# Kernel tuning notes

Measured on AMD Instinct MI355X. Metric: run time of the kernel, lower is better.

## Reference

```python
import jax, jax.numpy as jnp
import numpy as np

TEMPERATURE = 0.75
SINKHORN_ITERS = 7
EPS = 1e-6
R_THRESH = 1e-3


def setup_inputs() -> dict:
    key = jax.random.key(0)
    k1, k2, k3, k4 = jax.random.split(key, 4)
    b, h, t, d = 1, 8, 2048, 64
    n = 32  # uniform buckets of size t // n = 64
    q = jax.random.normal(k1, (b, h, t, d), jnp.float32)
    k_ = jax.random.normal(k2, (b, h, t, d), jnp.float32)
    v = jax.random.normal(k3, (b, h, t, d), jnp.float32)
    gumbel_u = jax.random.uniform(k4, (b * h, n, n), jnp.float32)
    return {"q": q, "k": k_, "v": v, "gumbel_u": gumbel_u, "num_buckets": n}


def _sort_net_R(qm, km, gumbel_u, d):
    # qm, km: [bh, n, s, d] -> bucket sums [bh, n, d]
    q_sums = qm.sum(axis=2)
    k_sums = km.sum(axis=2)
    logits = jnp.einsum('bie,bje->bij', q_sums, k_sums) * (d ** -0.5)
    # gumbel_sinkhorn(relu(logits))
    r = jnp.log(jax.nn.relu(logits) + EPS)
    g = -jnp.log(-jnp.log(gumbel_u + EPS) + EPS)
    r = (r + g) / TEMPERATURE
    for _ in range(SINKHORN_ITERS):
        r = r - jax.nn.logsumexp(r, axis=2, keepdims=True)
        r = r - jax.nn.logsumexp(r, axis=1, keepdims=True)
    return jnp.exp(r)  # [bh, n, n]


def reference(q, k, v, gumbel_u, num_buckets):
    b, h, t, d = q.shape
    bh = b * h
    n = num_buckets
    s = t // n  # uniform bucket size
    qm = q.reshape(bh, n, s, d)
    km = k.reshape(bh, n, s, d)
    vm = v.reshape(bh, n, s, d)

    R = _sort_net_R(qm, km, gumbel_u, d)
    # torch skips pairs with R_ij <= 1e-3 (output is zero); multiply by masked R
    Rm = jnp.where(R > R_THRESH, R, 0.0)

    scale = d ** -0.5
    # keys for pair (i, j) are concat(k_i, k_j): split score into self + cross
    S_self = jnp.einsum('bise,bite->bist', qm, km) * scale          # [bh,n,s,s]
    S_cross = jnp.einsum('bise,bjte->bijst', qm, km) * scale        # [bh,n,n,s,s]
    scores = jnp.concatenate(
        [jnp.broadcast_to(S_self[:, :, None], (bh, n, n, s, s)), S_cross],
        axis=-1)                                                    # [bh,n,n,s,2s]
    w = jax.nn.softmax(scores, axis=-1)
    w_i, w_j = w[..., :s], w[..., s:]
    # out_ij = (w_i @ v_i + w_j @ v_j) * R_ij, summed over j
    out = (jnp.einsum('bijst,bite,bij->bise', w_i, vm, Rm)
           + jnp.einsum('bijst,bjte,bij->bise', w_j, vm, Rm))       # [bh,n,s,d]
    return out.reshape(b, h, t, d)
```

## Files before the change

kernel.cpp:

```cpp
#include <hip/hip_runtime.h>
#include <math.h>
#include <stdint.h>

#define BH 8
#define NB 32
#define SS 64
#define DD 64
#define TT 2048

typedef float f32x16 __attribute__((ext_vector_type(16)));
typedef short bf16x8 __attribute__((ext_vector_type(8)));
typedef unsigned short u16;

__device__ __forceinline__ unsigned pkbf(float a, float b) {
  unsigned r;
  asm("v_cvt_pk_bf16_f32 %0, %1, %2" : "=v"(r) : "v"(a), "v"(b));
  return r;
}
__device__ __forceinline__ float exp2x(float x) {
  float r;
  asm("v_exp_f32 %0, %1" : "=v"(r) : "v"(x));
  return r;
}
__device__ __forceinline__ float log2x(float x) {
  float r;
  asm("v_log_f32 %0, %1" : "=v"(r) : "v"(x));
  return r;
}
__device__ __forceinline__ bf16x8 pack8v(const f32x16& v, const int b) {
  union { unsigned u[4]; bf16x8 v8; } x;
  x.u[0] = pkbf(v[b + 0], v[b + 1]);
  x.u[1] = pkbf(v[b + 2], v[b + 3]);
  x.u[2] = pkbf(v[b + 4], v[b + 5]);
  x.u[3] = pkbf(v[b + 6], v[b + 7]);
  return x.v8;
}

__global__ __launch_bounds__(256) void prep_kernel(
    const float* __restrict__ q, const float* __restrict__ k, const float* __restrict__ v,
    u16* __restrict__ qb, u16* __restrict__ kb, u16* __restrict__ vtb,
    float* __restrict__ qsum, float* __restrict__ ksum)
{
  __shared__ float qt[64][68];
  __shared__ float kt[64][68];
  __shared__ float vt[64][68];

  const int T = blockIdx.x;
  const int t = threadIdx.x;
  const float* qsrc = q + (size_t)T * 4096;
  const float* ksrc = k + (size_t)T * 4096;
  const float* vsrc = v + (size_t)T * 4096;

#pragma unroll
  for (int r4 = 0; r4 < 4; ++r4) {
    int f = r4 * 256 + t;
    int row = f >> 4, c4 = (f & 15) << 2;
    *(float4*)&qt[row][c4] = ((const float4*)qsrc)[f];
    *(float4*)&kt[row][c4] = ((const float4*)ksrc)[f];
    *(float4*)&vt[row][c4] = ((const float4*)vsrc)[f];
  }
  __syncthreads();

  const float qscale = 0.18033688011112042f;

#pragma unroll
  for (int half = 0; half < 2; ++half) {
    int x = half * 256 + t;
    int c = x >> 6, lane = x & 63;
    int l31 = lane & 31, hi = lane >> 5;
    int m = c >> 2, s = c & 3;
    int row = l31 + 32 * m;
    int cb = 16 * s + 4 * hi;
    float4 a = *(const float4*)&qt[row][cb];
    float4 b = *(const float4*)&qt[row][cb + 8];
    uint4 o;
    o.x = pkbf(a.x * qscale, a.y * qscale);
    o.y = pkbf(a.z * qscale, a.w * qscale);
    o.z = pkbf(b.x * qscale, b.y * qscale);
    o.w = pkbf(b.z * qscale, b.w * qscale);
    *(uint4*)(qb + (size_t)T * 4096 + (size_t)x * 8) = o;

    float4 ka = *(const float4*)&kt[row][cb];
    float4 kb4 = *(const float4*)&kt[row][cb + 8];
    uint4 ko;
    ko.x = pkbf(ka.x, ka.y);
    ko.y = pkbf(ka.z, ka.w);
    ko.z = pkbf(kb4.x, kb4.y);
    ko.w = pkbf(kb4.z, kb4.w);
    *(uint4*)(kb + (size_t)T * 4096 + (size_t)x * 8) = ko;

    int d = l31 + 32 * m;
    int kb0 = 16 * s + 4 * hi;
    uint4 vo;
    vo.x = pkbf(vt[kb0 + 0][d], vt[kb0 + 1][d]);
    vo.y = pkbf(vt[kb0 + 2][d], vt[kb0 + 3][d]);
    vo.z = pkbf(vt[kb0 + 8][d], vt[kb0 + 9][d]);
    vo.w = pkbf(vt[kb0 + 10][d], vt[kb0 + 11][d]);
    *(uint4*)(vtb + (size_t)T * 4096 + (size_t)x * 8) = vo;
  }

  if (t < 64) {
    float s = 0.f;
#pragma unroll 8
    for (int r = 0; r < 64; ++r) s += qt[r][t];
    qsum[T * 64 + t] = s;
  } else if (t < 128) {
    int c = t - 64;
    float s = 0.f;
#pragma unroll 8
    for (int r = 0; r < 64; ++r) s += kt[r][c];
    ksum[T * 64 + c] = s;
  }
}

__global__ __launch_bounds__(512) void attn_kernel(
    const u16* __restrict__ qb, const u16* __restrict__ kb,
    const u16* __restrict__ vtb, const float* __restrict__ qsum,
    const float* __restrict__ ksum, const float* __restrict__ gu,
    float* __restrict__ out)
{
  __shared__ __align__(16) unsigned char smem[35840];
  float (*redh)[2][32][68] = (float (*)[2][32][68])smem;
  float (*cbuf)[32] = (float (*)[32])(smem + 34816);
  float* qs    = (float*)smem;
  float* ks    = qs + 32 * 65;
  float* rbufS = ks + 32 * 65;
  float* colb  = rbufS + 32 * 33;
  float* RmRow = colb + 32;

  const int bh  = blockIdx.x & 7;
  const int i   = blockIdx.x >> 3;
  const int t   = threadIdx.x;
  const int w   = t >> 6;
  const int n   = w & 1;
  const int g   = w >> 1;
  const int lane = t & 63;
  const int l31 = lane & 31;
  const int hi  = lane >> 5;

  const u16* qtile = qb + ((size_t)(bh * NB + i)) * 4096;
  const u16* kbh   = kb + (size_t)bh * NB * 4096;
  const u16* vbh   = vtb + (size_t)bh * NB * 4096;

#define LOADG(dst, base)                                                      \
  {                                                                           \
    _Pragma("unroll") for (int m = 0; m < 2; ++m)                             \
    _Pragma("unroll") for (int s = 0; s < 4; ++s)                             \
      dst[m][s] = *(const bf16x8*)((base) + ((size_t)((m * 4 + s) * 64 + lane)) * 8); \
  }

  bf16x8 qB[4];
#pragma unroll
  for (int s = 0; s < 4; ++s)
    qB[s] = *(const bf16x8*)(qtile + ((size_t)((n * 4 + s) * 64 + lane)) * 8);

  float rij8[8];
  {
    const float L2E = 1.4426950408889634f;
    const float LN2 = 0.6931471805599453f;

    {
      int idx = t * 4;
      float4 qv = *(const float4*)(qsum + bh * 2048 + idx);
      float4 kv = *(const float4*)(ksum + bh * 2048 + idx);
      int b = idx >> 6, e = idx & 63;
      float* qd = qs + b * 65 + e;
      qd[0] = qv.x; qd[1] = qv.y; qd[2] = qv.z; qd[3] = qv.w;
      float* kd = ks + b * 65 + e;
      kd[0] = kv.x; kd[1] = kv.y; kd[2] = kv.z; kd[3] = kv.w;
    }
    __syncthreads();

    const int G = t >> 5;
    const int j = t & 31;
    float rr2[2];
#pragma unroll
    for (int x = 0; x < 2; ++x) {
      int ii = G + 16 * x;
      float acc = 0.f;
      for (int e = 0; e < 64; ++e) acc += qs[ii * 65 + e] * ks[j * 65 + e];
      acc *= 0.125f;
      float u = gu[bh * 1024 + ii * 32 + j];
      float gg = -logf(-logf(u + 1e-6f) + 1e-6f);
      rr2[x] = (logf(fmaxf(acc, 0.f) + 1e-6f) + gg) * (1.0f / 0.75f);
    }

    for (int it = 0; it < 7; ++it) {
#pragma unroll
      for (int x = 0; x < 2; ++x) {
        float s = exp2x(rr2[x] * L2E);
        s += __shfl_xor(s, 16, 32);
        s += __shfl_xor(s, 8, 32);
        s += __shfl_xor(s, 4, 32);
        s += __shfl_xor(s, 2, 32);
        s += __shfl_xor(s, 1, 32);
        rr2[x] -= log2x(fmaxf(s, 1e-30f)) * LN2;
      }
#pragma unroll
      for (int x = 0; x < 2; ++x) rbufS[(G + 16 * x) * 33 + j] = rr2[x];
      __syncthreads();
#pragma unroll
      for (int x = 0; x < 2; ++x) {
        int col = G + 16 * x;
        float s2 = exp2x(rbufS[j * 33 + col] * L2E);
        s2 += __shfl_xor(s2, 16, 32);
        s2 += __shfl_xor(s2, 8, 32);
        s2 += __shfl_xor(s2, 4, 32);
        s2 += __shfl_xor(s2, 2, 32);
        s2 += __shfl_xor(s2, 1, 32);
        if (j == 0) colb[col] = log2x(fmaxf(s2, 1e-30f)) * LN2;
      }
      __syncthreads();
#pragma unroll
      for (int x = 0; x < 2; ++x) rr2[x] -= colb[j];
    }

#pragma unroll
    for (int x = 0; x < 2; ++x) {
      if (G + 16 * x == i) {
        float R = exp2x(rr2[x] * L2E);
        RmRow[j] = (R > 1e-3f) ? R : 0.f;
      }
    }
    __syncthreads();
#pragma unroll
    for (int jj = 0; jj < 8; ++jj) rij8[jj] = RmRow[g + 4 * jj];
  }

  bf16x8 kA[2][4], vB[2][4];
  LOADG(kA, kbh + (size_t)g * 4096);
  LOADG(vB, vbh + (size_t)g * 4096);

  float m0, S0;
  bf16x8 psA[4];
  {
    const u16* kib = kbh + (size_t)i * 4096;
    bf16x8 kAi[2][4];
    LOADG(kAi, kib);
    f32x16 aS0, aS1;
#pragma unroll
    for (int r = 0; r < 16; ++r) { aS0[r] = 0.f; aS1[r] = 0.f; }
#pragma unroll
    for (int s = 0; s < 4; ++s) {
      aS0 = __builtin_amdgcn_mfma_f32_32x32x16_bf16(kAi[0][s], qB[s], aS0, 0, 0, 0);
      aS1 = __builtin_amdgcn_mfma_f32_32x32x16_bf16(kAi[1][s], qB[s], aS1, 0, 0, 0);
    }
    float mx[16];
#pragma unroll
    for (int r = 0; r < 16; ++r) mx[r] = fmaxf(aS0[r], aS1[r]);
#pragma unroll
    for (int off = 8; off > 0; off >>= 1)
#pragma unroll
      for (int r = 0; r < off; ++r) mx[r] = fmaxf(mx[r], mx[r + off]);
    float mm = fmaxf(mx[0], __shfl_xor(mx[0], 32, 64));
#pragma unroll
    for (int r = 0; r < 16; ++r) { aS0[r] = exp2x(aS0[r] - mm); aS1[r] = exp2x(aS1[r] - mm); }
    float sm[16];
#pragma unroll
    for (int r = 0; r < 16; ++r) sm[r] = aS0[r] + aS1[r];
#pragma unroll
    for (int off = 8; off > 0; off >>= 1)
#pragma unroll
      for (int r = 0; r < off; ++r) sm[r] += sm[r + off];
    S0 = sm[0] + __shfl_xor(sm[0], 32, 64);
    m0 = mm;
    psA[0] = pack8v(aS0, 0);
    psA[1] = pack8v(aS0, 8);
    psA[2] = pack8v(aS1, 0);
    psA[3] = pack8v(aS1, 8);
  }

  f32x16 outAcc[2];
#pragma unroll
  for (int nv = 0; nv < 2; ++nv)
#pragma unroll
    for (int e = 0; e < 16; ++e) outAcc[nv][e] = 0.f;
  float cacc = 0.f;

#pragma unroll
  for (int jj = 0; jj < 8; ++jj) {
    const int j = g + 4 * jj;
    const float rij = rij8[jj];

    f32x16 a0, a1;
#pragma unroll
    for (int r = 0; r < 16; ++r) { a0[r] = 0.f; a1[r] = 0.f; }
    __builtin_amdgcn_s_setprio(1);
#pragma unroll
    for (int s = 0; s < 4; ++s) {
      a0 = __builtin_amdgcn_mfma_f32_32x32x16_bf16(kA[0][s], qB[s], a0, 0, 0, 0);
      a1 = __builtin_amdgcn_mfma_f32_32x32x16_bf16(kA[1][s], qB[s], a1, 0, 0, 0);
    }
    __builtin_amdgcn_s_setprio(0);

    if (jj < 7) LOADG(kA, kbh + (size_t)(j + 4) * 4096);

    float mx[16];
#pragma unroll
    for (int r = 0; r < 16; ++r) mx[r] = fmaxf(a0[r], a1[r]);
#pragma unroll
    for (int off = 8; off > 0; off >>= 1)
#pragma unroll
      for (int r = 0; r < off; ++r) mx[r] = fmaxf(mx[r], mx[r + off]);
    float mc = fmaxf(mx[0], __shfl_xor(mx[0], 32, 64));
    float mj = fmaxf(m0, mc);
#pragma unroll
    for (int r = 0; r < 16; ++r) { a0[r] = exp2x(a0[r] - mj); a1[r] = exp2x(a1[r] - mj); }
    float sm[16];
#pragma unroll
    for (int r = 0; r < 16; ++r) sm[r] = a0[r] + a1[r];
#pragma unroll
    for (int off = 8; off > 0; off >>= 1)
#pragma unroll
      for (int r = 0; r < off; ++r) sm[r] += sm[r + off];
    float ssum = sm[0] + __shfl_xor(sm[0], 32, 64);
    float e0 = exp2x(m0 - mj);
    float den = S0 * e0 + ssum;
    float inv = rij / den;
    cacc += e0 * inv;
#pragma unroll
    for (int r = 0; r < 16; ++r) { a0[r] *= inv; a1[r] *= inv; }

    __builtin_amdgcn_s_setprio(1);
#pragma unroll
    for (int s = 0; s < 4; ++s) {
      bf16x8 wf = (s < 2) ? pack8v(a0, 8 * (s & 1)) : pack8v(a1, 8 * (s & 1));
      outAcc[0] = __builtin_amdgcn_mfma_f32_32x32x16_bf16(wf, vB[0][s], outAcc[0], 0, 0, 0);
      outAcc[1] = __builtin_amdgcn_mfma_f32_32x32x16_bf16(wf, vB[1][s], outAcc[1], 0, 0, 0);
    }
    __builtin_amdgcn_s_setprio(0);

    if (jj < 7) LOADG(vB, vbh + (size_t)(j + 4) * 4096);
  }

  {
    const u16* vib = vbh + (size_t)i * 4096;
    bf16x8 vBi[2][4];
    LOADG(vBi, vib);
    f32x16 U[2];
#pragma unroll
    for (int nv = 0; nv < 2; ++nv)
#pragma unroll
      for (int e = 0; e < 16; ++e) U[nv][e] = 0.f;
#pragma unroll
    for (int s = 0; s < 4; ++s) {
      U[0] = __builtin_amdgcn_mfma_f32_32x32x16_bf16(psA[s], vBi[0][s], U[0], 0, 0, 0);
      U[1] = __builtin_amdgcn_mfma_f32_32x32x16_bf16(psA[s], vBi[1][s], U[1], 0, 0, 0);
    }
    if (hi == 0) cbuf[w][l31] = cacc;
    __syncthreads();
#pragma unroll
    for (int r = 0; r < 16; ++r) {
      int row = (r & 3) + 8 * (r >> 2) + 4 * hi;
      float cr = cbuf[w][row];
      outAcc[0][r] += U[0][r] * cr;
      outAcc[1][r] += U[1][r] * cr;
    }
  }

#define RED_W(buf)                                                         \
  {                                                                        \
    _Pragma("unroll") for (int ne = 0; ne < 2; ++ne)                       \
    _Pragma("unroll") for (int r = 0; r < 16; ++r) {                       \
      int row = (r & 3) + 8 * (r >> 2) + 4 * hi;                           \
      (buf)[row][l31 + 32 * ne] = outAcc[ne][r];                           \
    }                                                                      \
  }
#define RED_A(buf)                                                         \
  {                                                                        \
    _Pragma("unroll") for (int ne = 0; ne < 2; ++ne)                       \
    _Pragma("unroll") for (int r = 0; r < 16; ++r) {                       \
      int row = (r & 3) + 8 * (r >> 2) + 4 * hi;                           \
      outAcc[ne][r] += (buf)[row][l31 + 32 * ne];                          \
    }                                                                      \
  }

  if (g >= 2) RED_W(redh[n][g - 2]);
  __syncthreads();
  if (g < 2) RED_A(redh[n][g]);
  __syncthreads();
  if (g == 1) RED_W(redh[n][0]);
  __syncthreads();
  if (g == 0) {
    RED_A(redh[n][0]);
    RED_W(redh[n][0]);
  }
  __syncthreads();

  {
    int row = t >> 3;
    int nr = row >> 5, lrow = row & 31;
    int col0 = (t & 7) * 8;
    float4 a = *(const float4*)&redh[nr][0][lrow][col0];
    float4 b = *(const float4*)&redh[nr][0][lrow][col0 + 4];
    float* ob = out + ((size_t)bh * TT + i * SS + row) * DD + col0;
    *(float4*)ob = a;
    *(float4*)(ob + 4) = b;
  }
#undef LOADG
#undef RED_W
#undef RED_A
}

extern "C" void kernel_launch(void* const* d_in, const int* in_sizes, int n_in,
                              void* d_out, int out_size, void* d_ws, size_t ws_size,
                              hipStream_t stream) {
  (void)in_sizes; (void)n_in; (void)out_size; (void)ws_size;
  const float* q  = (const float*)d_in[0];
  const float* k  = (const float*)d_in[1];
  const float* v  = (const float*)d_in[2];
  const float* gu = (const float*)d_in[3];
  float* out = (float*)d_out;

  char* wsb = (char*)d_ws;
  u16* qb   = (u16*)(wsb);
  u16* kb   = (u16*)(wsb + (1 << 21));
  u16* vtb  = (u16*)(wsb + (2 << 21));
  float* qsum = (float*)(wsb + (3 << 21));
  float* ksum = (float*)(wsb + (3 << 21) + (1 << 16));

  prep_kernel<<<256, 256, 0, stream>>>(q, k, v, qb, kb, vtb, qsum, ksum);
  attn_kernel<<<BH * NB, 512, 0, stream>>>(qb, kb, vtb, qsum, ksum, gu, out);
}
```

Before: 34.26 us.

## Compute Sinkhorn matrix once per head in extra prep blocks instead of per attention block

Measured after the change: 48.44 us. +41.4%, slower.

```diff
diff --git a/kernel.cpp b/kernel.cpp
--- a/kernel.cpp
+++ b/kernel.cpp
@@ -38,95 +38,185 @@
 
 __global__ __launch_bounds__(256) void prep_kernel(
     const float* __restrict__ q, const float* __restrict__ k, const float* __restrict__ v,
+    const float* __restrict__ gu,
     u16* __restrict__ qb, u16* __restrict__ kb, u16* __restrict__ vtb,
-    float* __restrict__ qsum, float* __restrict__ ksum)
+    float* __restrict__ qsum, float* __restrict__ ksum, float* __restrict__ Rm)
 {
-  __shared__ float qt[64][68];
-  __shared__ float kt[64][68];
-  __shared__ float vt[64][68];
-
-  const int T = blockIdx.x;
+  __shared__ float smemF[3][64][68];
+
+  const int bid = blockIdx.x;
   const int t = threadIdx.x;
-  const float* qsrc = q + (size_t)T * 4096;
-  const float* ksrc = k + (size_t)T * 4096;
-  const float* vsrc = v + (size_t)T * 4096;
-
-#pragma unroll
-  for (int r4 = 0; r4 < 4; ++r4) {
-    int f = r4 * 256 + t;
-    int row = f >> 4, c4 = (f & 15) << 2;
-    *(float4*)&qt[row][c4] = ((const float4*)qsrc)[f];
-    *(float4*)&kt[row][c4] = ((const float4*)ksrc)[f];
-    *(float4*)&vt[row][c4] = ((const float4*)vsrc)[f];
-  }
-  __syncthreads();
-
-  const float qscale = 0.18033688011112042f;
-
-#pragma unroll
-  for (int half = 0; half < 2; ++half) {
-    int x = half * 256 + t;
-    int c = x >> 6, lane = x & 63;
-    int l31 = lane & 31, hi = lane >> 5;
-    int m = c >> 2, s = c & 3;
-    int row = l31 + 32 * m;
-    int cb = 16 * s + 4 * hi;
-    float4 a = *(const float4*)&qt[row][cb];
-    float4 b = *(const float4*)&qt[row][cb + 8];
-    uint4 o;
-    o.x = pkbf(a.x * qscale, a.y * qscale);
-    o.y = pkbf(a.z * qscale, a.w * qscale);
-    o.z = pkbf(b.x * qscale, b.y * qscale);
-    o.w = pkbf(b.z * qscale, b.w * qscale);
-    *(uint4*)(qb + (size_t)T * 4096 + (size_t)x * 8) = o;
-
-    float4 ka = *(const float4*)&kt[row][cb];
-    float4 kb4 = *(const float4*)&kt[row][cb + 8];
-    uint4 ko;
-    ko.x = pkbf(ka.x, ka.y);
-    ko.y = pkbf(ka.z, ka.w);
-    ko.z = pkbf(kb4.x, kb4.y);
-    ko.w = pkbf(kb4.z, kb4.w);
-    *(uint4*)(kb + (size_t)T * 4096 + (size_t)x * 8) = ko;
-
-    int d = l31 + 32 * m;
-    int kb0 = 16 * s + 4 * hi;
-    uint4 vo;
-    vo.x = pkbf(vt[kb0 + 0][d], vt[kb0 + 1][d]);
-    vo.y = pkbf(vt[kb0 + 2][d], vt[kb0 + 3][d]);
-    vo.z = pkbf(vt[kb0 + 8][d], vt[kb0 + 9][d]);
-    vo.w = pkbf(vt[kb0 + 10][d], vt[kb0 + 11][d]);
-    *(uint4*)(vtb + (size_t)T * 4096 + (size_t)x * 8) = vo;
-  }
-
-  if (t < 64) {
-    float s = 0.f;
+
+  if (bid < 256) {
+    float (*qt)[68] = smemF[0];
+    float (*kt)[68] = smemF[1];
+    float (*vt)[68] = smemF[2];
+    const int T = bid;
+    const float* qsrc = q + (size_t)T * 4096;
+    const float* ksrc = k + (size_t)T * 4096;
+    const float* vsrc = v + (size_t)T * 4096;
+
+#pragma unroll
+    for (int r4 = 0; r4 < 4; ++r4) {
+      int f = r4 * 256 + t;
+      int row = f >> 4, c4 = (f & 15) << 2;
+      *(float4*)&qt[row][c4] = ((const float4*)qsrc)[f];
+      *(float4*)&kt[row][c4] = ((const float4*)ksrc)[f];
+      *(float4*)&vt[row][c4] = ((const float4*)vsrc)[f];
+    }
+    __syncthreads();
+
+    const float qscale = 0.18033688011112042f;
+
+#pragma unroll
+    for (int half = 0; half < 2; ++half) {
+      int x = half * 256 + t;
+      int c = x >> 6, lane = x & 63;
+      int l31 = lane & 31, hi = lane >> 5;
+      int m = c >> 2, s = c & 3;
+      int row = l31 + 32 * m;
+      int cb = 16 * s + 4 * hi;
+      float4 a = *(const float4*)&qt[row][cb];
+      float4 b = *(const float4*)&qt[row][cb + 8];
+      uint4 o;
+      o.x = pkbf(a.x * qscale, a.y * qscale);
+      o.y = pkbf(a.z * qscale, a.w * qscale);
+      o.z = pkbf(b.x * qscale, b.y * qscale);
+      o.w = pkbf(b.z * qscale, b.w * qscale);
+      *(uint4*)(qb + (size_t)T * 4096 + (size_t)x * 8) = o;
+
+      float4 ka = *(const float4*)&kt[row][cb];
+      float4 kb4 = *(const float4*)&kt[row][cb + 8];
+      uint4 ko;
+      ko.x = pkbf(ka.x, ka.y);
+      ko.y = pkbf(ka.z, ka.w);
+      ko.z = pkbf(kb4.x, kb4.y);
+      ko.w = pkbf(kb4.z, kb4.w);
+      *(uint4*)(kb + (size_t)T * 4096 + (size_t)x * 8) = ko;
+
+      int d = l31 + 32 * m;
+      int kb0 = 16 * s + 4 * hi;
+      uint4 vo;
+      vo.x = pkbf(vt[kb0 + 0][d], vt[kb0 + 1][d]);
+      vo.y = pkbf(vt[kb0 + 2][d], vt[kb0 + 3][d]);
+      vo.z = pkbf(vt[kb0 + 8][d], vt[kb0 + 9][d]);
+      vo.w = pkbf(vt[kb0 + 10][d], vt[kb0 + 11][d]);
+      *(uint4*)(vtb + (size_t)T * 4096 + (size_t)x * 8) = vo;
+    }
+
+    if (t < 64) {
+      float s = 0.f;
 #pragma unroll 8
-    for (int r = 0; r < 64; ++r) s += qt[r][t];
-    qsum[T * 64 + t] = s;
-  } else if (t < 128) {
-    int c = t - 64;
-    float s = 0.f;
+      for (int r = 0; r < 64; ++r) s += qt[r][t];
+      qsum[T * 64 + t] = s;
+    } else if (t < 128) {
+      int c = t - 64;
+      float s = 0.f;
 #pragma unroll 8
-    for (int r = 0; r < 64; ++r) s += kt[r][c];
-    ksum[T * 64 + c] = s;
+      for (int r = 0; r < 64; ++r) s += kt[r][c];
+      ksum[T * 64 + c] = s;
+    }
+  } else {
+    const int bh2 = bid - 256;
+    const float L2E = 1.4426950408889634f;
+    const float LN2 = 0.6931471805599453f;
+    float* qs = &smemF[0][0][0];
+    float* ks = qs + 32 * 65;
+    float* LT = ks + 32 * 65;
+
+    {
+      const int b = t >> 3;
+      const int d8 = (t & 7) * 8;
+      float sq[8], sk[8];
+#pragma unroll
+      for (int x = 0; x < 8; ++x) { sq[x] = 0.f; sk[x] = 0.f; }
+      const float* qpb = q + ((size_t)bh2 * 2048 + b * 64) * 64 + d8;
+      const float* kpb = k + ((size_t)bh2 * 2048 + b * 64) * 64 + d8;
+      for (int row = 0; row < 64; ++row) {
+        float4 a = *(const float4*)(qpb + row * 64);
+        float4 b4 = *(const float4*)(qpb + row * 64 + 4);
+        sq[0] += a.x; sq[1] += a.y; sq[2] += a.z; sq[3] += a.w;
+        sq[4] += b4.x; sq[5] += b4.y; sq[6] += b4.z; sq[7] += b4.w;
+        float4 c = *(const float4*)(kpb + row * 64);
+        float4 d4 = *(const float4*)(kpb + row * 64 + 4);
+        sk[0] += c.x; sk[1] += c.y; sk[2] += c.z; sk[3] += c.w;
+        sk[4] += d4.x; sk[5] += d4.y; sk[6] += d4.z; sk[7] += d4.w;
+      }
+#pragma unroll
+      for (int x = 0; x < 8; ++x) {
+        qs[b * 65 + d8 + x] = sq[x];
+        ks[b * 65 + d8 + x] = sk[x];
+      }
+    }
+    __syncthreads();
+
+    {
+      const int i0 = t >> 5, j = t & 31;
+#pragma unroll
+      for (int x = 0; x < 4; ++x) {
+        int ii = i0 + 8 * x;
+        float acc = 0.f;
+        for (int e = 0; e < 64; ++e) acc += qs[ii * 65 + e] * ks[j * 65 + e];
+        acc *= 0.125f;
+        float u = gu[bh2 * 1024 + ii * 32 + j];
+        float gg = -logf(-logf(u + 1e-6f) + 1e-6f);
+        LT[ii * 33 + j] = (logf(fmaxf(acc, 0.f) + 1e-6f) + gg) * (1.0f / 0.75f);
+      }
+    }
+    __syncthreads();
+
+    if (t < 32) {
+      const int l = t;
+      float r[32];
+#pragma unroll
+      for (int jj = 0; jj < 32; ++jj) r[jj] = LT[l * 33 + jj];
+
+      for (int it = 0; it < 7; ++it) {
+        {
+          float s = 0.f;
+#pragma unroll
+          for (int jj = 0; jj < 32; ++jj) s += exp2x(r[jj] * L2E);
+          float L = log2x(fmaxf(s, 1e-30f)) * LN2;
+#pragma unroll
+          for (int jj = 0; jj < 32; ++jj) r[jj] -= L;
+        }
+#pragma unroll
+        for (int jj = 0; jj < 32; ++jj) LT[l * 33 + jj] = r[jj];
+#pragma unroll
+        for (int jj = 0; jj < 32; ++jj) r[jj] = LT[jj * 33 + l];
+        {
+          float s = 0.f;
+#pragma unroll
+          for (int jj = 0; jj < 32; ++jj) s += exp2x(r[jj] * L2E);
+          float L = log2x(fmaxf(s, 1e-30f)) * LN2;
+#pragma unroll
+          for (int jj = 0; jj < 32; ++jj) r[jj] -= L;
+        }
+        if (it < 6) {
+#pragma unroll
+          for (int jj = 0; jj < 32; ++jj) LT[l * 33 + jj] = r[jj];
+#pragma unroll
+          for (int jj = 0; jj < 32; ++jj) r[jj] = LT[jj * 33 + l];
+        }
+      }
+
+#pragma unroll
+      for (int i = 0; i < 32; ++i) {
+        float R = exp2x(r[i] * L2E);
+        Rm[bh2 * 1024 + i * 32 + l] = (R > 1e-3f) ? R : 0.f;
+      }
+    }
   }
 }
 
 __global__ __launch_bounds__(512) void attn_kernel(
     const u16* __restrict__ qb, const u16* __restrict__ kb,
-    const u16* __restrict__ vtb, const float* __restrict__ qsum,
-    const float* __restrict__ ksum, const float* __restrict__ gu,
+    const u16* __restrict__ vtb, const float* __restrict__ Rm,
     float* __restrict__ out)
 {
   __shared__ __align__(16) unsigned char smem[35840];
   float (*redh)[2][32][68] = (float (*)[2][32][68])smem;
   float (*cbuf)[32] = (float (*)[32])(smem + 34816);
-  float* qs    = (float*)smem;
-  float* ks    = qs + 32 * 65;
-  float* rbufS = ks + 32 * 65;
-  float* colb  = rbufS + 32 * 33;
-  float* RmRow = colb + 32;
 
   const int bh  = blockIdx.x & 7;
   const int i   = blockIdx.x >> 3;
@@ -149,83 +239,14 @@
       dst[m][s] = *(const bf16x8*)((base) + ((size_t)((m * 4 + s) * 64 + lane)) * 8); \
   }
 
+  float rij8[8];
+#pragma unroll
+  for (int jj = 0; jj < 8; ++jj) rij8[jj] = Rm[bh * 1024 + i * 32 + g + 4 * jj];
+
   bf16x8 qB[4];
 #pragma unroll
   for (int s = 0; s < 4; ++s)
     qB[s] = *(const bf16x8*)(qtile + ((size_t)((n * 4 + s) * 64 + lane)) * 8);
-
-  float rij8[8];
-  {
-    const float L2E = 1.4426950408889634f;
-    const float LN2 = 0.6931471805599453f;
-
-    {
-      int idx = t * 4;
-      float4 qv = *(const float4*)(qsum + bh * 2048 + idx);
-      float4 kv = *(const float4*)(ksum + bh * 2048 + idx);
-      int b = idx >> 6, e = idx & 63;
-      float* qd = qs + b * 65 + e;
-      qd[0] = qv.x; qd[1] = qv.y; qd[2] = qv.z; qd[3] = qv.w;
-      float* kd = ks + b * 65 + e;
-      kd[0] = kv.x; kd[1] = kv.y; kd[2] = kv.z; kd[3] = kv.w;
-    }
-    __syncthreads();
-
-    const int G = t >> 5;
-    const int j = t & 31;
-    float rr2[2];
-#pragma unroll
-    for (int x = 0; x < 2; ++x) {
-      int ii = G + 16 * x;
-      float acc = 0.f;
-      for (int e = 0; e < 64; ++e) acc += qs[ii * 65 + e] * ks[j * 65 + e];
-      acc *= 0.125f;
-      float u = gu[bh * 1024 + ii * 32 + j];
-      float gg = -logf(-logf(u + 1e-6f) + 1e-6f);
-      rr2[x] = (logf(fmaxf(acc, 0.f) + 1e-6f) + gg) * (1.0f / 0.75f);
-    }
-
-    for (int it = 0; it < 7; ++it) {
-#pragma unroll
-      for (int x = 0; x < 2; ++x) {
-        float s = exp2x(rr2[x] * L2E);
-        s += __shfl_xor(s, 16, 32);
-        s += __shfl_xor(s, 8, 32);
-        s += __shfl_xor(s, 4, 32);
-        s += __shfl_xor(s, 2, 32);
-        s += __shfl_xor(s, 1, 32);
-        rr2[x] -= log2x(fmaxf(s, 1e-30f)) * LN2;
-      }
-#pragma unroll
-      for (int x = 0; x < 2; ++x) rbufS[(G + 16 * x) * 33 + j] = rr2[x];
-      __syncthreads();
-#pragma unroll
-      for (int x = 0; x < 2; ++x) {
-        int col = G + 16 * x;
-        float s2 = exp2x(rbufS[j * 33 + col] * L2E);
-        s2 += __shfl_xor(s2, 16, 32);
-        s2 += __shfl_xor(s2, 8, 32);
-        s2 += __shfl_xor(s2, 4, 32);
-        s2 += __shfl_xor(s2, 2, 32);
-        s2 += __shfl_xor(s2, 1, 32);
-        if (j == 0) colb[col] = log2x(fmaxf(s2, 1e-30f)) * LN2;
-      }
-      __syncthreads();
-#pragma unroll
-      for (int x = 0; x < 2; ++x) rr2[x] -= colb[j];
-    }
-
-#pragma unroll
-    for (int x = 0; x < 2; ++x) {
-      if (G + 16 * x == i) {
-        float R = exp2x(rr2[x] * L2E);
-        RmRow[j] = (R > 1e-3f) ? R : 0.f;
-      }
-    }
-    __syncthreads();
-#pragma unroll
-    for (int jj = 0; jj < 8; ++jj) rij8[jj] = RmRow[g + 4 * jj];
-  }
 
   bf16x8 kA[2][4], vB[2][4];
   LOADG(kA, kbh + (size_t)g * 4096);
@@ -418,7 +439,8 @@
   u16* vtb  = (u16*)(wsb + (2 << 21));
   float* qsum = (float*)(wsb + (3 << 21));
   float* ksum = (float*)(wsb + (3 << 21) + (1 << 16));
-
-  prep_kernel<<<256, 256, 0, stream>>>(q, k, v, qb, kb, vtb, qsum, ksum);
-  attn_kernel<<<BH * NB, 512, 0, stream>>>(qb, kb, vtb, qsum, ksum, gu, out);
-}
+  float* Rm   = (float*)(wsb + (3 << 21) + (2 << 16));
+
+  prep_kernel<<<264, 256, 0, stream>>>(q, k, v, gu, qb, kb, vtb, qsum, ksum, Rm);
+  attn_kernel<<<BH * NB, 512, 0, stream>>>(qb, kb, vtb, Rm, out);
+}
```
